# Kernel optimization log

Hardware: AMD Instinct MI355X
Metric: run time of the kernel (lower is better)

The kernel has to match this reference:

```python
import jax, jax.numpy as jnp
import numpy as np

B, T, E, H, HS, L, V = 128, 256, 384, 6, 64, 6, 78
FF = 4 * E  # 1536


def layer_norm(x, g, b, eps=1e-5):
    mu = jnp.mean(x, axis=-1, keepdims=True)
    var = jnp.mean((x - mu) ** 2, axis=-1, keepdims=True)
    return (x - mu) * jax.lax.rsqrt(var + eps) * g + b


def setup_inputs() -> dict:
    key = jax.random.key(0)
    ks = jax.random.split(key, 20)
    s = 0.02
    return {
        "context": jax.random.randint(ks[0], (B, T), 0, V),
        "tok_emb": jax.random.normal(ks[1], (V, E)) * s,
        "pos_emb": jax.random.normal(ks[2], (T, E)) * s,
        "ln1_g": jnp.ones((L, E)), "ln1_b": jnp.zeros((L, E)),
        "w_qkv": jax.random.normal(ks[3], (L, H, E, 3 * HS)) * s,  # per-head qkv, no bias
        "w_proj": jax.random.normal(ks[4], (L, E, E)) * s,
        "b_proj": jnp.zeros((L, E)),
        "ln2_g": jnp.ones((L, E)), "ln2_b": jnp.zeros((L, E)),
        "w1": jax.random.normal(ks[5], (L, E, FF)) * s, "b1": jnp.zeros((L, FF)),
        "w2": jax.random.normal(ks[6], (L, FF, E)) * s, "b2": jnp.zeros((L, E)),
        "lnf_g": jnp.ones((E,)), "lnf_b": jnp.zeros((E,)),
        "w_head": jax.random.normal(ks[7], (E, V)) * s, "b_head": jnp.zeros((V,)),
    }


def reference(context, tok_emb, pos_emb, ln1_g, ln1_b, w_qkv, w_proj, b_proj,
              ln2_g, ln2_b, w1, b1, w2, b2, lnf_g, lnf_b, w_head, b_head):
    x = tok_emb[context] + pos_emb[None, :, :]            # [B,T,E]
    causal = jnp.tril(jnp.ones((T, T), dtype=bool))       # lower-tri mask
    scale = HS ** (-0.5)
    for l in range(L):
        # multi-head attention (pre-LN), per-head qkv projection, no bias
        xn = layer_norm(x, ln1_g[l], ln1_b[l])
        qkv = jnp.einsum('bte,hef->bthf', xn, w_qkv[l])   # [B,T,H,3*HS]
        q, k, v = jnp.split(qkv, 3, axis=-1)              # each [B,T,H,HS]
        scores = jnp.einsum('bthd,bshd->bhts', q, k) * scale
        scores = jnp.where(causal, scores, -jnp.inf)
        att = jax.nn.softmax(scores, axis=-1)             # [B,H,T,T]
        o = jnp.einsum('bhts,bshd->bthd', att, v).reshape(B, T, E)
        x = x + o @ w_proj[l] + b_proj[l]
        # feed-forward (pre-LN)
        xn2 = layer_norm(x, ln2_g[l], ln2_b[l])
        x = x + jax.nn.relu(xn2 @ w1[l] + b1[l]) @ w2[l] + b2[l]
    x = layer_norm(x, lnf_g, lnf_b)
    return x @ w_head + b_head                            # [B,T,V]
```

## Files before the change

### kernel.cpp

```cpp
#include <hip/hip_runtime.h>


#define Bc 128
#define Tc 256
#define Ec 384
#define Hc 6
#define HSc 64
#define Lc 6
#define Vc 78
#define FFc 1536
#define Mc (Bc * Tc)

typedef unsigned short u16;
using bf16x8 = __attribute__((ext_vector_type(8))) short;
using f32x4 = __attribute__((ext_vector_type(4))) float;

__device__ __forceinline__ float b2f(u16 u) {
    union { float f; unsigned int i; } x;
    x.i = ((unsigned int)u) << 16;
    return x.f;
}
__device__ __forceinline__ u16 f2b(float f) {
    union { float f; unsigned int u; } x;
    x.f = f;
    unsigned int r = x.u + 0x7fffu + ((x.u >> 16) & 1u);
    return (u16)(r >> 16);
}

__device__ __forceinline__ void gload_lds16(const u16* g, u16* l) {
    __builtin_amdgcn_global_load_lds(
        (const __attribute__((address_space(1))) unsigned int*)g,
        (__attribute__((address_space(3))) unsigned int*)l, 16, 0, 0);
}

__global__ __launch_bounds__(256) void poison_kernel(
    float* __restrict__ out, int n, float val) {
    int i = blockIdx.x * 256 + threadIdx.x;
    if (i < n) out[i] = val;
}

__global__ __launch_bounds__(256) void trans_qkv_kernel(
    const float* __restrict__ in, u16* __restrict__ out) {
    int i = blockIdx.x * 256 + threadIdx.x;
    if (i >= Lc * Hc * Ec * 192) return;
    int f = i % 192;
    int r = i / 192;
    int e = r % Ec; r /= Ec;
    int h = r % Hc;
    int l = r / Hc;
    out[((size_t)l * 1152 + h * 192 + f) * Ec + e] = f2b(in[i]);
}
__global__ __launch_bounds__(256) void trans_w_kernel(
    const float* __restrict__ in, u16* __restrict__ out, int K, int N) {
    int i = blockIdx.x * 256 + threadIdx.x;
    if (i >= Lc * K * N) return;
    int n = i % N;
    int r = i / N;
    int k = r % K;
    int l = r / K;
    out[((size_t)l * N + n) * K + k] = f2b(in[i]);
}
__global__ __launch_bounds__(256) void trans_head_kernel(
    const float* __restrict__ in, u16* __restrict__ out) {
    int i = blockIdx.x * 256 + threadIdx.x;
    if (i >= Ec * Vc) return;
    int v = i % Vc, e = i / Vc;
    out[(size_t)v * Ec + e] = f2b(in[i]);
}

__global__ __launch_bounds__(256) void embed_kernel(
    const int* __restrict__ ctx, const float* __restrict__ tok,
    const float* __restrict__ pos, float* __restrict__ x) {
    int i = blockIdx.x * 256 + threadIdx.x;
    if (i >= Mc * 96) return;
    int c4 = (i % 96) * 4, bt = i / 96, t = bt % Tc;
    f32x4 tv = *reinterpret_cast<const f32x4*>(&tok[ctx[bt] * Ec + c4]);
    f32x4 pv = *reinterpret_cast<const f32x4*>(&pos[t * Ec + c4]);
    *reinterpret_cast<f32x4*>(&x[(size_t)bt * Ec + c4]) = tv + pv;
}

__global__ __launch_bounds__(256) void ln_kernel(
    const float* __restrict__ X, u16* __restrict__ Y,
    const float* __restrict__ g, const float* __restrict__ b, int nrows) {
    int row = blockIdx.x * 4 + (threadIdx.x >> 6);
    int lane = threadIdx.x & 63;
    if (row >= nrows) return;
    const float* xr = X + (size_t)row * Ec;
    float2 v[3];
    float s = 0.f;
#pragma unroll
    for (int i = 0; i < 3; ++i) {
        v[i] = *reinterpret_cast<const float2*>(&xr[2 * lane + 128 * i]);
        s += v[i].x + v[i].y;
    }
#pragma unroll
    for (int off = 32; off >= 1; off >>= 1) s += __shfl_xor(s, off, 64);
    float mean = s * (1.0f / Ec);
    float s2 = 0.f;
#pragma unroll
    for (int i = 0; i < 3; ++i) {
        float dx = v[i].x - mean, dy = v[i].y - mean;
        s2 += dx * dx + dy * dy;
    }
#pragma unroll
    for (int off = 32; off >= 1; off >>= 1) s2 += __shfl_xor(s2, off, 64);
    float rstd = rsqrtf(s2 * (1.0f / Ec) + 1e-5f);
    u16* yr = Y + (size_t)row * Ec;
#pragma unroll
    for (int i = 0; i < 3; ++i) {
        int e = 2 * lane + 128 * i;
        float2 gv = *reinterpret_cast<const float2*>(&g[e]);
        float2 bv = *reinterpret_cast<const float2*>(&b[e]);
        ushort2 ov;
        ov.x = f2b((v[i].x - mean) * rstd * gv.x + bv.x);
        ov.y = f2b((v[i].y - mean) * rstd * gv.y + bv.y);
        *reinterpret_cast<ushort2*>(&yr[e]) = ov;
    }
}

template <bool RELU, bool RESID, bool OUTBF16, bool VECEPI>
__global__ __launch_bounds__(256) void mfma_gemm(
    const u16* __restrict__ A, const u16* __restrict__ Wt,
    const float* __restrict__ bias, const float* R, void* C,
    int K, int ldC, int NV) {
    constexpr bool SWAP = VECEPI && !OUTBF16;
    __shared__ __align__(16) u16 smem[128 * 128];
    u16(*As)[64] = (u16(*)[64])smem;
    u16(*Bs)[64] = (u16(*)[64])(smem + 128 * 64);
    int tid = threadIdx.x;

    int nwg = gridDim.x * gridDim.y;
    int bid = blockIdx.y * gridDim.x + blockIdx.x;
    int q = nwg >> 3, r = nwg & 7;
    int xcd = bid & 7, idx = bid >> 3;
    int swz = (xcd < r ? xcd * (q + 1) : r * (q + 1) + (xcd - r) * q) + idx;
    int bx = swz % gridDim.x, by = swz / gridDim.x;
    int m0 = by * 128, n0 = bx * 128;

    int w = tid >> 6, lane = tid & 63;
    int wm = (w >> 1) * 64, wn = (w & 1) * 64;
    int r16 = lane & 15, quad = lane >> 4;

    int lrow = lane >> 3;
    int scol = ((lane & 7) ^ lrow) * 8;
    const u16* ap[4];
    const u16* bp[4];
#pragma unroll
    for (int j = 0; j < 4; ++j) {
        int row = (w * 4 + j) * 8 + lrow;
        ap[j] = A + (size_t)(m0 + row) * K + scol;
        bp[j] = Wt + (size_t)(n0 + row) * K + scol;
    }

    f32x4 acc[4][4] = {};

    for (int k0 = 0; k0 < K; k0 += 64) {
        __syncthreads();
#pragma unroll
        for (int j = 0; j < 4; ++j) {
            gload_lds16(ap[j], &As[(w * 4 + j) * 8][0]);
            gload_lds16(bp[j], &Bs[(w * 4 + j) * 8][0]);
            ap[j] += 64;
            bp[j] += 64;
        }
        __syncthreads();
#pragma unroll
        for (int kk = 0; kk < 2; ++kk) {
            int csw = ((kk * 4 + quad) ^ (r16 & 7)) * 8;
            bf16x8 af[4], bf[4];
#pragma unroll
            for (int i = 0; i < 4; ++i) {
                af[i] = *reinterpret_cast<const bf16x8*>(
                    &As[wm + i * 16 + r16][csw]);
                bf[i] = *reinterpret_cast<const bf16x8*>(
                    &Bs[wn + i * 16 + r16][csw]);
            }
#pragma unroll
            for (int mi = 0; mi < 4; ++mi)
#pragma unroll
                for (int ni = 0; ni < 4; ++ni) {
                    if (SWAP)
                        acc[mi][ni] = __builtin_amdgcn_mfma_f32_16x16x32_bf16(
                            bf[ni], af[mi], acc[mi][ni], 0, 0, 0);
                    else
                        acc[mi][ni] = __builtin_amdgcn_mfma_f32_16x16x32_bf16(
                            af[mi], bf[ni], acc[mi][ni], 0, 0, 0);
                }
        }
    }

    if (VECEPI && OUTBF16) {
        float bv[4];
#pragma unroll
        for (int ni = 0; ni < 4; ++ni)
            bv[ni] = bias ? bias[n0 + wn + ni * 16 + r16] : 0.f;
        __syncthreads();
#pragma unroll
        for (int mi = 0; mi < 4; ++mi)
#pragma unroll
            for (int ni = 0; ni < 4; ++ni)
#pragma unroll
                for (int reg = 0; reg < 4; ++reg) {
                    int row = wm + mi * 16 + quad * 4 + reg;
                    int col = wn + ni * 16 + r16;
                    float v = acc[mi][ni][reg] + bv[ni];
                    if (RELU) v = fmaxf(v, 0.f);
                    int pc = (col >> 3) ^ (row & 15);
                    smem[row * 128 + pc * 8 + (col & 7)] = f2b(v);
                }
        __syncthreads();
        u16* cp = (u16*)C;
#pragma unroll
        for (int i = 0; i < 4; ++i) {
            int row = (tid >> 3) + 32 * i;
#pragma unroll
            for (int h = 0; h < 2; ++h) {
                int lc = (tid & 7) + 8 * h;
                int pc = lc ^ (row & 15);
                bf16x8 val = *reinterpret_cast<const bf16x8*>(
                    &smem[row * 128 + pc * 8]);
                *reinterpret_cast<bf16x8*>(
                    &cp[(size_t)(m0 + row) * ldC + n0 + lc * 8]) = val;
            }
        }
    } else if (VECEPI) {
        float* cp = (float*)C;
        f32x4 bv4[4];
#pragma unroll
        for (int ni = 0; ni < 4; ++ni) {
            int gn = n0 + wn + ni * 16 + quad * 4;
            if (bias)
                bv4[ni] = *reinterpret_cast<const f32x4*>(&bias[gn]);
            else
                bv4[ni] = f32x4{0.f, 0.f, 0.f, 0.f};
        }
#pragma unroll
        for (int mi = 0; mi < 4; ++mi) {
            int gm = m0 + wm + mi * 16 + r16;
#pragma unroll
            for (int ni = 0; ni < 4; ++ni) {
                int gn = n0 + wn + ni * 16 + quad * 4;
                size_t goff = (size_t)gm * ldC + gn;
                f32x4 v = acc[mi][ni] + bv4[ni];
                if (RELU) {
#pragma unroll
                    for (int e = 0; e < 4; ++e) v[e] = fmaxf(v[e], 0.f);
                }
                if (RESID) v += *reinterpret_cast<const f32x4*>(&R[goff]);
                *reinterpret_cast<f32x4*>(&cp[goff]) = v;
            }
        }
    } else {
#pragma unroll
        for (int mi = 0; mi < 4; ++mi)
#pragma unroll
            for (int ni = 0; ni < 4; ++ni) {
                int gn = n0 + wn + ni * 16 + r16;
                if (gn >= NV) continue;
                float bvs = bias ? bias[gn] : 0.f;
#pragma unroll
                for (int reg = 0; reg < 4; ++reg) {
                    int gm = m0 + wm + mi * 16 + quad * 4 + reg;
                    float v = acc[mi][ni][reg] + bvs;
                    if (RESID) v += R[(size_t)gm * ldC + gn];
                    if (RELU) v = fmaxf(v, 0.f);
                    if (OUTBF16)
                        ((u16*)C)[(size_t)gm * ldC + gn] = f2b(v);
                    else
                        ((float*)C)[(size_t)gm * ldC + gn] = v;
                }
            }
    }
}

__global__ __launch_bounds__(256) void attn_kernel(
    const u16* __restrict__ qkv, u16* __restrict__ o) {
    __shared__ u16 Qs[64][72];
    __shared__ u16 Ks[64][72];
    __shared__ u16 Vt[64][72];
    __shared__ u16 Ps[4][16][72];
    int tid = threadIdx.x;
    int tt = blockIdx.x, h = blockIdx.y, b = blockIdx.z;
    int w = tid >> 6, lane = tid & 63;
    int r16 = lane & 15, quad = lane >> 4;
    int t0 = tt * 64;
    const u16* base = qkv + (size_t)b * Tc * 1152 + h * 192;

    int sr = tid >> 2, sd = (tid & 3) * 16;
    {
        const u16* src = base + (size_t)(t0 + sr) * 1152 + sd;
        *reinterpret_cast<uint4*>(&Qs[sr][sd]) =
            *reinterpret_cast<const uint4*>(src);
        *reinterpret_cast<uint4*>(&Qs[sr][sd + 8]) =
            *reinterpret_cast<const uint4*>(src + 8);
    }
    __syncthreads();
    bf16x8 aq0 = *reinterpret_cast<const bf16x8*>(&Qs[w * 16 + r16][quad * 8]);
    bf16x8 aq1 = *reinterpret_cast<const bf16x8*>(&Qs[w * 16 + r16][32 + quad * 8]);

    uint4 kr0, kr1, vr0, vr1;
    {
        const u16* ks = base + (size_t)sr * 1152 + 64 + sd;
        kr0 = *reinterpret_cast<const uint4*>(ks);
        kr1 = *reinterpret_cast<const uint4*>(ks + 8);
        const u16* vs = base + (size_t)sr * 1152 + 128 + sd;
        vr0 = *reinterpret_cast<const uint4*>(vs);
        vr1 = *reinterpret_cast<const uint4*>(vs + 8);
    }

    float m_run[4], l_run[4];
#pragma unroll
    for (int r = 0; r < 4; ++r) { m_run[r] = -3.0e38f; l_run[r] = 0.f; }
    f32x4 acc_o[4] = {};

    for (int st = 0; st <= tt; ++st) {
        __syncthreads();
        {
            *reinterpret_cast<uint4*>(&Ks[sr][sd]) = kr0;
            *reinterpret_cast<uint4*>(&Ks[sr][sd + 8]) = kr1;
            u16 tv[16];
            *reinterpret_cast<uint4*>(tv) = vr0;
            *reinterpret_cast<uint4*>(tv + 8) = vr1;
#pragma unroll
            for (int j = 0; j < 16; ++j) Vt[sd + j][sr] = tv[j];
        }
        __syncthreads();
        if (st < tt) {
            const u16* ks = base + (size_t)((st + 1) * 64 + sr) * 1152 + 64 + sd;
            kr0 = *reinterpret_cast<const uint4*>(ks);
            kr1 = *reinterpret_cast<const uint4*>(ks + 8);
            const u16* vs = base + (size_t)((st + 1) * 64 + sr) * 1152 + 128 + sd;
            vr0 = *reinterpret_cast<const uint4*>(vs);
            vr1 = *reinterpret_cast<const uint4*>(vs + 8);
        }

        f32x4 acc_s[4] = {};
#pragma unroll
        for (int ni = 0; ni < 4; ++ni) {
            bf16x8 bk0 = *reinterpret_cast<const bf16x8*>(&Ks[ni * 16 + r16][quad * 8]);
            bf16x8 bk1 = *reinterpret_cast<const bf16x8*>(&Ks[ni * 16 + r16][32 + quad * 8]);
            acc_s[ni] = __builtin_amdgcn_mfma_f32_16x16x32_bf16(aq0, bk0, acc_s[ni], 0, 0, 0);
            acc_s[ni] = __builtin_amdgcn_mfma_f32_16x16x32_bf16(aq1, bk1, acc_s[ni], 0, 0, 0);
        }

        float sc[4][4];
        float mt[4] = {-3.0e38f, -3.0e38f, -3.0e38f, -3.0e38f};
#pragma unroll
        for (int ni = 0; ni < 4; ++ni)
#pragma unroll
            for (int reg = 0; reg < 4; ++reg) {
                int col = st * 64 + ni * 16 + r16;
                int row = t0 + w * 16 + quad * 4 + reg;
                float v = (col <= row) ? acc_s[ni][reg] * 0.125f : -3.0e38f;
                sc[ni][reg] = v;
                mt[reg] = fmaxf(mt[reg], v);
            }
#pragma unroll
        for (int reg = 0; reg < 4; ++reg) {
#pragma unroll
            for (int off = 1; off <= 8; off <<= 1)
                mt[reg] = fmaxf(mt[reg], __shfl_xor(mt[reg], off, 64));
        }
        float alpha[4], lt[4];
#pragma unroll
        for (int reg = 0; reg < 4; ++reg) {
            float m_new = fmaxf(m_run[reg], mt[reg]);
            alpha[reg] = __expf(m_run[reg] - m_new);
            m_run[reg] = m_new;
            lt[reg] = 0.f;
        }
#pragma unroll
        for (int ni = 0; ni < 4; ++ni)
#pragma unroll
            for (int reg = 0; reg < 4; ++reg) {
                float p = __expf(sc[ni][reg] - m_run[reg]);
                lt[reg] += p;
                Ps[w][quad * 4 + reg][ni * 16 + r16] = f2b(p);
            }
#pragma unroll
        for (int reg = 0; reg < 4; ++reg) {
#pragma unroll
            for (int off = 1; off <= 8; off <<= 1)
                lt[reg] += __shfl_xor(lt[reg], off, 64);
            l_run[reg] = l_run[reg] * alpha[reg] + lt[reg];
        }
#pragma unroll
        for (int ni = 0; ni < 4; ++ni)
#pragma unroll
            for (int reg = 0; reg < 4; ++reg) acc_o[ni][reg] *= alpha[reg];
        __syncthreads();

        bf16x8 ap0 = *reinterpret_cast<const bf16x8*>(&Ps[w][r16][quad * 8]);
        bf16x8 ap1 = *reinterpret_cast<const bf16x8*>(&Ps[w][r16][32 + quad * 8]);
#pragma unroll
        for (int ni = 0; ni < 4; ++ni) {
            bf16x8 bv0 = *reinterpret_cast<const bf16x8*>(&Vt[ni * 16 + r16][quad * 8]);
            bf16x8 bv1 = *reinterpret_cast<const bf16x8*>(&Vt[ni * 16 + r16][32 + quad * 8]);
            acc_o[ni] = __builtin_amdgcn_mfma_f32_16x16x32_bf16(ap0, bv0, acc_o[ni], 0, 0, 0);
            acc_o[ni] = __builtin_amdgcn_mfma_f32_16x16x32_bf16(ap1, bv1, acc_o[ni], 0, 0, 0);
        }
    }

    float inv[4];
#pragma unroll
    for (int reg = 0; reg < 4; ++reg) inv[reg] = 1.0f / l_run[reg];
#pragma unroll
    for (int ni = 0; ni < 4; ++ni)
#pragma unroll
        for (int reg = 0; reg < 4; ++reg) {
            int t = t0 + w * 16 + quad * 4 + reg;
            o[((size_t)b * Tc + t) * Ec + h * 64 + ni * 16 + r16] =
                f2b(acc_o[ni][reg] * inv[reg]);
        }
}

#define GRD(n) dim3(((n) + 255) / 256)

extern "C" void kernel_launch(void* const* d_in, const int* in_sizes, int n_in,
                              void* d_out, int out_size, void* d_ws, size_t ws_size,
                              hipStream_t stream) {
    const int* ctx = (const int*)d_in[0];
    const float* tok = (const float*)d_in[1];
    const float* pos = (const float*)d_in[2];
    const float* ln1g = (const float*)d_in[3];
    const float* ln1b = (const float*)d_in[4];
    const float* wqkv = (const float*)d_in[5];
    const float* wproj = (const float*)d_in[6];
    const float* bproj = (const float*)d_in[7];
    const float* ln2g = (const float*)d_in[8];
    const float* ln2b = (const float*)d_in[9];
    const float* w1 = (const float*)d_in[10];
    const float* b1 = (const float*)d_in[11];
    const float* w2 = (const float*)d_in[12];
    const float* b2 = (const float*)d_in[13];
    const float* lnfg = (const float*)d_in[14];
    const float* lnfb = (const float*)d_in[15];
    const float* whead = (const float*)d_in[16];
    const float* bhead = (const float*)d_in[17];
    float* out = (float*)d_out;

    char* ws = (char*)d_ws;
    float* x = (float*)ws;
    size_t off = (size_t)Mc * Ec * 4;
    u16* wqkvT = (u16*)(ws + off); off += (size_t)Lc * 1152 * 384 * 2;
    u16* wprojT = (u16*)(ws + off); off += (size_t)Lc * 384 * 384 * 2;
    u16* w1T = (u16*)(ws + off); off += (size_t)Lc * 1536 * 384 * 2;
    u16* w2T = (u16*)(ws + off); off += (size_t)Lc * 384 * 1536 * 2;
    u16* wheadT = (u16*)(ws + off); off += (size_t)128 * 384 * 2;
    const size_t per_b = (size_t)Tc * (Ec + 1152 + Ec + FFc) * 2;
    if (ws_size < off + per_b) {
        poison_kernel<<<GRD(out_size), 256, 0, stream>>>(out, out_size, 200.0f);
        return;
    }
    int CB = (int)((ws_size - off) / per_b);
    if (CB > Bc) CB = Bc;
    u16* xn_c = (u16*)(ws + off);
    u16* qkv_c = xn_c + (size_t)CB * Tc * Ec;
    u16* o_c = qkv_c + (size_t)CB * Tc * 1152;
    u16* ff_c = o_c + (size_t)CB * Tc * Ec;

    trans_qkv_kernel<<<GRD(Lc * Hc * Ec * 192), 256, 0, stream>>>(wqkv, wqkvT);
    trans_w_kernel<<<GRD(Lc * Ec * Ec), 256, 0, stream>>>(wproj, wprojT, Ec, Ec);
    trans_w_kernel<<<GRD(Lc * Ec * FFc), 256, 0, stream>>>(w1, w1T, Ec, FFc);
    trans_w_kernel<<<GRD(Lc * FFc * Ec), 256, 0, stream>>>(w2, w2T, FFc, Ec);
    hipMemsetAsync(wheadT, 0, (size_t)128 * 384 * 2, stream);
    trans_head_kernel<<<GRD(Ec * Vc), 256, 0, stream>>>(whead, wheadT);

    embed_kernel<<<GRD(Mc * 96), 256, 0, stream>>>(ctx, tok, pos, x);

    for (int l = 0; l < Lc; ++l) {
        for (int b0 = 0; b0 < Bc; b0 += CB) {
            int bcnt = (Bc - b0 < CB) ? (Bc - b0) : CB;
            int rows = bcnt * Tc;
            float* xc = x + (size_t)b0 * Tc * Ec;
            ln_kernel<<<rows / 4, 256, 0, stream>>>(
                xc, xn_c, ln1g + l * Ec, ln1b + l * Ec, rows);
            mfma_gemm<false, false, true, true><<<dim3(1152 / 128, rows / 128), 256, 0, stream>>>(
                xn_c, wqkvT + (size_t)l * 1152 * 384, nullptr, nullptr, qkv_c,
                384, 1152, 1152);
            attn_kernel<<<dim3(Tc / 64, Hc, bcnt), 256, 0, stream>>>(qkv_c, o_c);
            mfma_gemm<false, true, false, true><<<dim3(Ec / 128, rows / 128), 256, 0, stream>>>(
                o_c, wprojT + (size_t)l * 384 * 384, bproj + l * Ec, xc, xc,
                384, Ec, Ec);
            ln_kernel<<<rows / 4, 256, 0, stream>>>(
                xc, xn_c, ln2g + l * Ec, ln2b + l * Ec, rows);
            mfma_gemm<true, false, true, true><<<dim3(FFc / 128, rows / 128), 256, 0, stream>>>(
                xn_c, w1T + (size_t)l * 1536 * 384, b1 + l * FFc, nullptr, ff_c,
                384, FFc, FFc);
            mfma_gemm<false, true, false, true><<<dim3(Ec / 128, rows / 128), 256, 0, stream>>>(
                ff_c, w2T + (size_t)l * 384 * 1536, b2 + l * Ec, xc, xc,
                1536, Ec, Ec);
        }
    }
    for (int b0 = 0; b0 < Bc; b0 += CB) {
        int bcnt = (Bc - b0 < CB) ? (Bc - b0) : CB;
        int rows = bcnt * Tc;
        float* xc = x + (size_t)b0 * Tc * Ec;
        ln_kernel<<<rows / 4, 256, 0, stream>>>(xc, xn_c, lnfg, lnfb, rows);
        mfma_gemm<false, false, false, false><<<dim3(1, rows / 128), 256, 0, stream>>>(
            xn_c, wheadT, bhead, nullptr, out + (size_t)b0 * Tc * Vc,
            384, Vc, Vc);
    }
}
```

Baseline: 2.319 ms.

## Add triple-buffered async LDS pipeline for the FFN down-projection GEMM

Adds a PIPE3 variant of the MFMA GEMM that uses three 32-wide K-slice LDS buffers, issuing global-to-LDS loads two steps ahead and waiting with explicit vmcnt counts, so loads overlap with MFMA compute. Only the K=1536 w2 GEMM enables it; the other GEMMs keep the old single-buffer 64-wide loop. The aim is to hide global load latency that the previous sync-load-sync-compute loop exposed. In exchange it uses more shared memory per block and smaller K steps with two barriers each, which may lower occupancy or add sync overhead.

```diff
diff --git a/kernel.cpp b/kernel.cpp
--- a/kernel.cpp
+++ b/kernel.cpp
@@ -118,15 +118,13 @@
     }
 }
 
-template <bool RELU, bool RESID, bool OUTBF16, bool VECEPI>
+template <bool RELU, bool RESID, bool OUTBF16, bool VECEPI, bool PIPE3>
 __global__ __launch_bounds__(256) void mfma_gemm(
     const u16* __restrict__ A, const u16* __restrict__ Wt,
     const float* __restrict__ bias, const float* R, void* C,
     int K, int ldC, int NV) {
     constexpr bool SWAP = VECEPI && !OUTBF16;
-    __shared__ __align__(16) u16 smem[128 * 128];
-    u16(*As)[64] = (u16(*)[64])smem;
-    u16(*Bs)[64] = (u16(*)[64])(smem + 128 * 64);
+    __shared__ __align__(16) u16 smem[PIPE3 ? 24576 : 16384];
     int tid = threadIdx.x;
 
     int nwg = gridDim.x * gridDim.y;
@@ -141,39 +139,34 @@
     int wm = (w >> 1) * 64, wn = (w & 1) * 64;
     int r16 = lane & 15, quad = lane >> 4;
 
-    int lrow = lane >> 3;
-    int scol = ((lane & 7) ^ lrow) * 8;
-    const u16* ap[4];
-    const u16* bp[4];
-#pragma unroll
-    for (int j = 0; j < 4; ++j) {
-        int row = (w * 4 + j) * 8 + lrow;
-        ap[j] = A + (size_t)(m0 + row) * K + scol;
-        bp[j] = Wt + (size_t)(n0 + row) * K + scol;
-    }
-
     f32x4 acc[4][4] = {};
 
-    for (int k0 = 0; k0 < K; k0 += 64) {
-        __syncthreads();
-#pragma unroll
-        for (int j = 0; j < 4; ++j) {
-            gload_lds16(ap[j], &As[(w * 4 + j) * 8][0]);
-            gload_lds16(bp[j], &Bs[(w * 4 + j) * 8][0]);
-            ap[j] += 64;
-            bp[j] += 64;
-        }
-        __syncthreads();
-#pragma unroll
-        for (int kk = 0; kk < 2; ++kk) {
-            int csw = ((kk * 4 + quad) ^ (r16 & 7)) * 8;
+    if constexpr (PIPE3) {
+        u16(*As3)[128][32] = (u16(*)[128][32])smem;
+        u16(*Bs3)[128][32] = (u16(*)[128][32])(smem + 3 * 128 * 32);
+        int rA = 2 * w * 16 + (lane >> 2);
+        int colsw = ((lane & 3) ^ ((lane >> 3) & 3)) * 8;
+        const u16* a0 = A + (size_t)(m0 + rA) * K + colsw;
+        const u16* a1 = A + (size_t)(m0 + rA + 16) * K + colsw;
+        const u16* b0 = Wt + (size_t)(n0 + rA) * K + colsw;
+        const u16* b1 = Wt + (size_t)(n0 + rA + 16) * K + colsw;
+
+        auto stage3 = [&](int buf, int t) {
+            int k0 = t * 32;
+            gload_lds16(a0 + k0, &As3[buf][2 * w * 16][0]);
+            gload_lds16(a1 + k0, &As3[buf][2 * w * 16 + 16][0]);
+            gload_lds16(b0 + k0, &Bs3[buf][2 * w * 16][0]);
+            gload_lds16(b1 + k0, &Bs3[buf][2 * w * 16 + 16][0]);
+        };
+        int csw = (quad ^ ((r16 >> 1) & 3)) * 8;
+        auto compute3 = [&](int buf) {
             bf16x8 af[4], bf[4];
 #pragma unroll
             for (int i = 0; i < 4; ++i) {
                 af[i] = *reinterpret_cast<const bf16x8*>(
-                    &As[wm + i * 16 + r16][csw]);
+                    &As3[buf][wm + i * 16 + r16][csw]);
                 bf[i] = *reinterpret_cast<const bf16x8*>(
-                    &Bs[wn + i * 16 + r16][csw]);
+                    &Bs3[buf][wn + i * 16 + r16][csw]);
             }
 #pragma unroll
             for (int mi = 0; mi < 4; ++mi)
@@ -186,6 +179,76 @@
                         acc[mi][ni] = __builtin_amdgcn_mfma_f32_16x16x32_bf16(
                             af[mi], bf[ni], acc[mi][ni], 0, 0, 0);
                 }
+        };
+
+        int nt = K >> 5;
+        stage3(0, 0);
+        stage3(1, 1);
+        int buf = 0;
+        for (int t = 0; t < nt - 1; ++t) {
+            asm volatile("s_waitcnt vmcnt(4)" ::: "memory");
+            __builtin_amdgcn_s_barrier();
+            __builtin_amdgcn_sched_barrier(0);
+            compute3(buf);
+            __builtin_amdgcn_s_barrier();
+            __builtin_amdgcn_sched_barrier(0);
+            if (t + 2 < nt) {
+                int b2 = buf + 2;
+                if (b2 >= 3) b2 -= 3;
+                stage3(b2, t + 2);
+            }
+            buf = (buf == 2) ? 0 : buf + 1;
+        }
+        asm volatile("s_waitcnt vmcnt(0)" ::: "memory");
+        __builtin_amdgcn_s_barrier();
+        __builtin_amdgcn_sched_barrier(0);
+        compute3(buf);
+    } else {
+        u16(*As)[64] = (u16(*)[64])smem;
+        u16(*Bs)[64] = (u16(*)[64])(smem + 128 * 64);
+        int lrow = lane >> 3;
+        int scol = ((lane & 7) ^ lrow) * 8;
+        const u16* ap[4];
+        const u16* bp[4];
+#pragma unroll
+        for (int j = 0; j < 4; ++j) {
+            int row = (w * 4 + j) * 8 + lrow;
+            ap[j] = A + (size_t)(m0 + row) * K + scol;
+            bp[j] = Wt + (size_t)(n0 + row) * K + scol;
+        }
+        for (int k0 = 0; k0 < K; k0 += 64) {
+            __syncthreads();
+#pragma unroll
+            for (int j = 0; j < 4; ++j) {
+                gload_lds16(ap[j], &As[(w * 4 + j) * 8][0]);
+                gload_lds16(bp[j], &Bs[(w * 4 + j) * 8][0]);
+                ap[j] += 64;
+                bp[j] += 64;
+            }
+            __syncthreads();
+#pragma unroll
+            for (int kk = 0; kk < 2; ++kk) {
+                int csw = ((kk * 4 + quad) ^ (r16 & 7)) * 8;
+                bf16x8 af[4], bf[4];
+#pragma unroll
+                for (int i = 0; i < 4; ++i) {
+                    af[i] = *reinterpret_cast<const bf16x8*>(
+                        &As[wm + i * 16 + r16][csw]);
+                    bf[i] = *reinterpret_cast<const bf16x8*>(
+                        &Bs[wn + i * 16 + r16][csw]);
+                }
+#pragma unroll
+                for (int mi = 0; mi < 4; ++mi)
+#pragma unroll
+                    for (int ni = 0; ni < 4; ++ni) {
+                        if (SWAP)
+                            acc[mi][ni] = __builtin_amdgcn_mfma_f32_16x16x32_bf16(
+                                bf[ni], af[mi], acc[mi][ni], 0, 0, 0);
+                        else
+                            acc[mi][ni] = __builtin_amdgcn_mfma_f32_16x16x32_bf16(
+                                af[mi], bf[ni], acc[mi][ni], 0, 0, 0);
+                    }
+            }
         }
     }
 
@@ -475,19 +538,19 @@
             float* xc = x + (size_t)b0 * Tc * Ec;
             ln_kernel<<<rows / 4, 256, 0, stream>>>(
                 xc, xn_c, ln1g + l * Ec, ln1b + l * Ec, rows);
-            mfma_gemm<false, false, true, true><<<dim3(1152 / 128, rows / 128), 256, 0, stream>>>(
+            mfma_gemm<false, false, true, true, false><<<dim3(1152 / 128, rows / 128), 256, 0, stream>>>(
                 xn_c, wqkvT + (size_t)l * 1152 * 384, nullptr, nullptr, qkv_c,
                 384, 1152, 1152);
             attn_kernel<<<dim3(Tc / 64, Hc, bcnt), 256, 0, stream>>>(qkv_c, o_c);
-            mfma_gemm<false, true, false, true><<<dim3(Ec / 128, rows / 128), 256, 0, stream>>>(
+            mfma_gemm<false, true, false, true, false><<<dim3(Ec / 128, rows / 128), 256, 0, stream>>>(
                 o_c, wprojT + (size_t)l * 384 * 384, bproj + l * Ec, xc, xc,
                 384, Ec, Ec);
             ln_kernel<<<rows / 4, 256, 0, stream>>>(
                 xc, xn_c, ln2g + l * Ec, ln2b + l * Ec, rows);
-            mfma_gemm<true, false, true, true><<<dim3(FFc / 128, rows / 128), 256, 0, stream>>>(
+            mfma_gemm<true, false, true, true, false><<<dim3(FFc / 128, rows / 128), 256, 0, stream>>>(
                 xn_c, w1T + (size_t)l * 1536 * 384, b1 + l * FFc, nullptr, ff_c,
                 384, FFc, FFc);
-            mfma_gemm<false, true, false, true><<<dim3(Ec / 128, rows / 128), 256, 0, stream>>>(
+            mfma_gemm<false, true, false, true, true><<<dim3(Ec / 128, rows / 128), 256, 0, stream>>>(
                 ff_c, w2T + (size_t)l * 384 * 1536, b2 + l * Ec, xc, xc,
                 1536, Ec, Ec);
         }
@@ -497,7 +560,7 @@
         int rows = bcnt * Tc;
         float* xc = x + (size_t)b0 * Tc * Ec;
         ln_kernel<<<rows / 4, 256, 0, stream>>>(xc, xn_c, lnfg, lnfb, rows);
-        mfma_gemm<false, false, false, false><<<dim3(1, rows / 128), 256, 0, stream>>>(
+        mfma_gemm<false, false, false, false, false><<<dim3(1, rows / 128), 256, 0, stream>>>(
             xn_c, wheadT, bhead, nullptr, out + (size_t)b0 * Tc * Vc,
             384, Vc, Vc);
     }
```

Measured after the change: 2.288 ms. No clear change (-1.3%).
